# Optimization experiments

Measured on AMD Instinct MI355X. Metric: run time of the kernel, lower is better.

The kernel has to match this reference:

```python
import jax, jax.numpy as jnp
import numpy as np

ES = 256
NUM_SPECIES, NUM_ABILITIES, NUM_ITEMS, NUM_MOVES = 1026, 300, 500, 920
NUM_ITEM_EFFECTS, NUM_GENDERS, NUM_STATUS, NUM_VOLATILE_STATUS = 16, 3, 8, 105
B, N, F = 8192, 12, 42
# feature layout (flat int32 vector per entity)
(SPECIES, ABILITY, ITEM, ITEM_EFFECT, GENDER, STATUS, BEING_CALLED_BACK, TRAPPED,
 NEWLY_SWITCHED, TOXIC_TURNS, SLEEP_TURNS, FAINTED, ACTIVE, SIDE, LEVEL, HP, MAXHP) = range(17)
BOOST0, VOL0, MOVEID0, MOVEPP0 = 17, 24, 33, 37  # 7 boosts, 9 volatile words, 4 moves, 4 pp

DENSE_DIMS = [("hp", 10), ("level", 7), ("active", 2), ("onehot", 32), ("boosts", 7),
              ("volatiles", NUM_VOLATILE_STATUS), ("item", ES + NUM_ITEM_EFFECTS),
              ("side", 2), ("moves", ES + 6)]

def _bits(x, world_dim):
    # binary-scale embedding: bit decomposition of an int feature
    nb = (world_dim - 1).bit_length()
    mask = jnp.asarray(1 << np.arange(nb), dtype=jnp.int32)
    return ((x[..., None] & mask) != 0).astype(jnp.float32)

def setup_inputs() -> dict:
    key = jax.random.key(0)
    ks = jax.random.split(key, 32)
    s = 0.02
    inp = {"entities": jax.random.randint(ks[0], (B, N, F), 0, 2, dtype=jnp.int32)}
    inp["embed_species"] = jax.random.normal(ks[1], (NUM_SPECIES, ES), jnp.float32) * s
    inp["embed_ability"] = jax.random.normal(ks[2], (NUM_ABILITIES, ES), jnp.float32) * s
    inp["embed_item"] = jax.random.normal(ks[3], (NUM_ITEMS, ES), jnp.float32) * s
    inp["embed_moves"] = jax.random.normal(ks[4], (NUM_MOVES, ES), jnp.float32) * s
    for i, (name, din) in enumerate(DENSE_DIMS):
        inp[f"{name}_W"] = jax.random.normal(ks[5 + i], (din, ES), jnp.float32) * s
        inp[f"{name}_b"] = jnp.zeros((ES,), jnp.float32)
    return inp

def _forward(entities, embed_species, embed_ability, embed_item, embed_moves,
             hp_W, hp_b, level_W, level_b, active_W, active_b, onehot_W, onehot_b,
             boosts_W, boosts_b, volatiles_W, volatiles_b, item_W, item_b,
             side_W, side_b, moves_W, moves_b):
    e = entities
    oh = jax.nn.one_hot
    dense = lambda x, W, b: x @ W + b
    hp = e[..., HP].astype(jnp.float32)
    maxhp = jnp.clip(e[..., MAXHP], 1).astype(jnp.float32)
    hp_ratio = jnp.clip(hp / maxhp, 0.0, 1.0)                      # (B,N)
    hp_token = jnp.floor(1023.0 * hp_ratio).astype(jnp.int32)
    boolean_code = jnp.concatenate([
        hp_ratio[..., None], oh(e[..., GENDER], NUM_GENDERS), oh(e[..., STATUS], NUM_STATUS),
        oh(e[..., BEING_CALLED_BACK], 2), oh(e[..., TRAPPED], 2), oh(e[..., NEWLY_SWITCHED], 2),
        oh(e[..., TOXIC_TURNS], 8), oh(e[..., SLEEP_TURNS], 4), oh(e[..., FAINTED], 2)], axis=-1)  # (B,N,32)
    item_onehot = jnp.concatenate([embed_item[e[..., ITEM]], oh(e[..., ITEM_EFFECT], NUM_ITEM_EFFECTS)], axis=-1)
    boosts = e[..., BOOST0:VOL0].astype(jnp.float32) / 2.0          # (B,N,7)
    vol = e[..., VOL0:VOL0 + 9]
    vbits = (vol[..., None] & jnp.arange(16)) > 0                   # (B,N,9,16)
    vol_oh = vbits.reshape(*vol.shape[:-1], 144)[..., :NUM_VOLATILE_STATUS].astype(jnp.float32)
    moveset = jnp.concatenate([embed_moves[e[..., MOVEID0:MOVEPP0]],
                               _bits(e[..., MOVEPP0:MOVEPP0 + 4], 64)], axis=-1)  # (B,N,4,262)
    moves_out = jnp.einsum('bnmf,fd->bnd', moveset, moves_W) + 4.0 * moves_b      # sum of 4 Dense outputs
    emb = (dense(_bits(hp_token, 1024), hp_W, hp_b)
           + dense(_bits(e[..., LEVEL], 101), level_W, level_b)
           + dense(oh(e[..., ACTIVE], 2), active_W, active_b)
           + dense(boolean_code, onehot_W, onehot_b)
           + dense(boosts, boosts_W, boosts_b)
           + dense(vol_oh, volatiles_W, volatiles_b)
           + embed_species[e[..., SPECIES]]
           + embed_ability[e[..., ABILITY]]
           + dense(item_onehot, item_W, item_b)
           + dense(oh(e[..., SIDE], 2), side_W, side_b)
           + moves_out)
    return emb

def reference(entities, embed_species, embed_ability, embed_item, embed_moves,
              hp_W, hp_b, level_W, level_b, active_W, active_b, onehot_W, onehot_b,
              boosts_W, boosts_b, volatiles_W, volatiles_b, item_W, item_b,
              side_W, side_b, moves_W, moves_b):
    return _forward(entities, embed_species, embed_ability, embed_item, embed_moves,
                    hp_W, hp_b, level_W, level_b, active_W, active_b, onehot_W, onehot_b,
                    boosts_W, boosts_b, volatiles_W, volatiles_b, item_W, item_b,
                    side_W, side_b, moves_W, moves_b)
```

## Files before the change

kernel.cpp:

```cpp
#include <hip/hip_runtime.h>

#define ES 256
#define B_DIM 8192
#define N_DIM 12
#define NFEAT 42
#define NENT (B_DIM * N_DIM)

#define F_SPECIES 0
#define F_ABILITY 1
#define F_ITEM 2
#define F_ITEM_EFFECT 3
#define F_GENDER 4
#define F_STATUS 5
#define F_BCB 6
#define F_TRAPPED 7
#define F_NEWSW 8
#define F_TOXIC 9
#define F_SLEEP 10
#define F_FAINTED 11
#define F_ACTIVE 12
#define F_SIDE 13
#define F_LEVEL 14
#define F_HP 15
#define F_MAXHP 16
#define F_BOOST0 17
#define F_VOL0 24
#define F_MOVEID0 33
#define F_MOVEPP0 37

#define OFF_HP     0
#define OFF_LV     (OFF_HP + 1024*ES)
#define OFF_PP     (OFF_LV + 128*ES)
#define OFF_VP     (OFF_PP + 64*ES)
#define OFF_CA     (OFF_VP + 784*ES)
#define OFF_CB     (OFF_CA + 768*ES)
#define OFF_EITEM  (OFF_CB + 1024*ES)
#define OFF_EMOVES (OFF_EITEM + 500*ES)
#define WS_FLOATS  (OFF_EMOVES + 920*ES)

#define TB_HP0 0
#define TB_LV0 1024
#define TB_PP0 1152
#define TB_VP0 1216
#define TB_CA0 2000
#define TB_CB0 2768
#define TB_EI0 3792
#define TB_EM0 3917
#define TB_TOT 4147

__global__ __launch_bounds__(256) void k_tables(
    const float* __restrict__ item_e, const float* __restrict__ moves_e,
    const float* __restrict__ hp_W, const float* __restrict__ level_W,
    const float* __restrict__ moves_W, const float* __restrict__ vol_W,
    const float* __restrict__ item_W, const float* __restrict__ onehot_W,
    const float* __restrict__ active_W, const float* __restrict__ side_W,
    const float* __restrict__ hp_b, const float* __restrict__ level_b,
    const float* __restrict__ active_b, const float* __restrict__ onehot_b,
    const float* __restrict__ boosts_b, const float* __restrict__ vol_b,
    const float* __restrict__ item_b, const float* __restrict__ side_b,
    const float* __restrict__ moves_b,
    float* __restrict__ ws) {
    __shared__ float se[4][ES];
    int bid = blockIdx.x;
    int d = threadIdx.x;

    if (bid < TB_LV0) {
        int v = bid;
        float acc = 0.f;
        for (int b = 0; b < 10; ++b)
            if ((v >> b) & 1) acc += hp_W[b * ES + d];
        ws[OFF_HP + v * ES + d] = acc;
    } else if (bid < TB_PP0) {
        int v = bid - TB_LV0;
        float acc = 0.f;
        for (int b = 0; b < 7; ++b)
            if ((v >> b) & 1) acc += level_W[b * ES + d];
        ws[OFF_LV + v * ES + d] = acc;
    } else if (bid < TB_VP0) {
        int v = bid - TB_PP0;
        float acc = 0.f;
        for (int b = 0; b < 6; ++b)
            if ((v >> b) & 1) acc += moves_W[(256 + b) * ES + d];
        ws[OFF_PP + v * ES + d] = acc;
    } else if (bid < TB_CA0) {
        int v = bid - TB_VP0;
        float acc = 0.f;
        if (v < 768) {
            int t = v >> 8, pair = v & 255, a = pair >> 4, b = pair & 15;
            for (int j = 0; j < 16; ++j) {
                if (a & j) acc += vol_W[(32 * t + j) * ES + d];
                if (b & j) acc += vol_W[(32 * t + 16 + j) * ES + d];
            }
        } else {
            int a = v - 768;
            for (int j = 0; j < 9; ++j)
                if (a & j) acc += vol_W[(96 + j) * ES + d];
        }
        ws[OFF_VP + v * ES + d] = acc;
    } else if (bid < TB_CB0) {
        int idx = bid - TB_CA0;
        int fa = idx & 1, ns = (idx >> 1) & 1, tr = (idx >> 2) & 1, bcb = (idx >> 3) & 1;
        int rest = idx >> 4, g = rest % 3, e = rest / 3;
        ws[OFF_CA + idx * ES + d] =
            item_W[(256 + e) * ES + d] + onehot_W[(1 + g) * ES + d] +
            onehot_W[(12 + bcb) * ES + d] + onehot_W[(14 + tr) * ES + d] +
            onehot_W[(16 + ns) * ES + d] + onehot_W[(30 + fa) * ES + d];
    } else if (bid < TB_EI0) {
        int idx = bid - TB_CB0;
        int sd = idx & 1, act = (idx >> 1) & 1, sl = (idx >> 2) & 3,
            tox = (idx >> 4) & 7, st = idx >> 7;
        float bias = hp_b[d] + level_b[d] + active_b[d] + onehot_b[d] + boosts_b[d] +
                     vol_b[d] + item_b[d] + side_b[d] + 4.0f * moves_b[d];
        ws[OFF_CB + idx * ES + d] =
            bias + onehot_W[(4 + st) * ES + d] + onehot_W[(18 + tox) * ES + d] +
            onehot_W[(26 + sl) * ES + d] + active_W[act * ES + d] + side_W[sd * ES + d];
    } else {
        const float* E; const float* W; float* o; int r0;
        if (bid < TB_EM0) { E = item_e;  W = item_W;  o = ws + OFF_EITEM;  r0 = (bid - TB_EI0) * 4; }
        else              { E = moves_e; W = moves_W; o = ws + OFF_EMOVES; r0 = (bid - TB_EM0) * 4; }
        for (int i = d; i < 4 * ES; i += 256)
            se[i >> 8][i & 255] = E[(r0 + (i >> 8)) * ES + (i & 255)];
        __syncthreads();
        int rl = d >> 6, lane = d & 63, d0 = lane * 4;
        float4 acc = make_float4(0.f, 0.f, 0.f, 0.f);
#pragma unroll 4
        for (int k = 0; k < ES; ++k) {
            float e = se[rl][k];
            const float4 w = *reinterpret_cast<const float4*>(&W[k * ES + d0]);
            acc.x += e * w.x; acc.y += e * w.y; acc.z += e * w.z; acc.w += e * w.w;
        }
        *reinterpret_cast<float4*>(&o[(r0 + rl) * ES + d0]) = acc;
    }
}


__device__ __forceinline__ float4 ld4(const float* p) {
    return *reinterpret_cast<const float4*>(p);
}
__device__ __forceinline__ void add4(float4& a, const float4 b) {
    a.x += b.x; a.y += b.y; a.z += b.z; a.w += b.w;
}
__device__ __forceinline__ void fma4(float4& a, float s, const float4 b) {
    a.x += s * b.x; a.y += s * b.y; a.z += s * b.z; a.w += s * b.w;
}
__device__ __forceinline__ int sclamp(int x, int lo, int hi) {
    return x < lo ? lo : (x > hi ? hi : x);
}

__global__ __launch_bounds__(256) void k_main(
    const int* __restrict__ ent,
    const float* __restrict__ spW, const float* __restrict__ abW,
    const float* __restrict__ onehotW, const float* __restrict__ boostsW,
    const float* __restrict__ ws,
    float* __restrict__ out) {
    int lane = threadIdx.x & 63;
    int wid  = (blockIdx.x * 256 + threadIdx.x) >> 6;
    int went = __builtin_amdgcn_readfirstlane(wid);
    int d0 = lane * 4;

    int fv = ent[went * NFEAT + (lane < NFEAT ? lane : 0)];
#define RL(i) __builtin_amdgcn_readlane(fv, (i))

    const float* Hp     = ws + OFF_HP;
    const float* Lv     = ws + OFF_LV;
    const float* Pp     = ws + OFF_PP;
    const float* VP     = ws + OFF_VP;
    const float* CA     = ws + OFF_CA;
    const float* CB     = ws + OFF_CB;
    const float* Eitem  = ws + OFF_EITEM;
    const float* Emoves = ws + OFF_EMOVES;

    int idxB = ((((RL(F_STATUS) & 7) * 8 + (RL(F_TOXIC) & 7)) * 4 + (RL(F_SLEEP) & 3)) * 2 +
                (RL(F_ACTIVE) & 1)) * 2 + (RL(F_SIDE) & 1);
    float4 acc = ld4(CB + idxB * ES + d0);

    int g = sclamp(RL(F_GENDER), 0, 2);
    int idxA = (((((RL(F_ITEM_EFFECT) & 15) * 3 + g) * 2 + (RL(F_BCB) & 1)) * 2 +
                 (RL(F_TRAPPED) & 1)) * 2 + (RL(F_NEWSW) & 1)) * 2 + (RL(F_FAINTED) & 1);
    add4(acc, ld4(CA + idxA * ES + d0));

    add4(acc, ld4(spW    + sclamp(RL(F_SPECIES), 0, 1025) * ES + d0));
    add4(acc, ld4(abW    + sclamp(RL(F_ABILITY), 0, 299)  * ES + d0));
    add4(acc, ld4(Eitem  + sclamp(RL(F_ITEM),    0, 499)  * ES + d0));

    {
        float hp = (float)RL(F_HP);
        int mh = RL(F_MAXHP); if (mh < 1) mh = 1;
        float ratio = fminf(fmaxf(hp / (float)mh, 0.f), 1.f);
        int tok = __builtin_amdgcn_readfirstlane((int)floorf(1023.f * ratio));
        add4(acc, ld4(Hp + tok * ES + d0));
        fma4(acc, ratio, ld4(onehotW + d0));
    }

    add4(acc, ld4(Lv + (RL(F_LEVEL) & 127) * ES + d0));

#pragma unroll
    for (int k = 0; k < 7; ++k) {
        int bv = RL(F_BOOST0 + k);
        if (bv != 0) fma4(acc, 0.5f * (float)bv, ld4(boostsW + k * ES + d0));
    }

#pragma unroll
    for (int t = 0; t < 3; ++t) {
        int pair = ((RL(F_VOL0 + 2 * t) & 15) << 4) | (RL(F_VOL0 + 2 * t + 1) & 15);
        if (pair != 0) add4(acc, ld4(VP + (t * 256 + pair) * ES + d0));
    }
    {
        int nib = RL(F_VOL0 + 6) & 15;
        if (nib != 0) add4(acc, ld4(VP + (768 + nib) * ES + d0));
    }

#pragma unroll
    for (int m = 0; m < 4; ++m) {
        add4(acc, ld4(Emoves + sclamp(RL(F_MOVEID0 + m), 0, 919) * ES + d0));
        int pp = RL(F_MOVEPP0 + m) & 63;
        if (pp != 0) add4(acc, ld4(Pp + pp * ES + d0));
    }
#undef RL

    *reinterpret_cast<float4*>(&out[went * ES + d0]) = acc;
}


extern "C" void kernel_launch(void* const* d_in, const int* in_sizes, int n_in,
                              void* d_out, int out_size, void* d_ws, size_t ws_size,
                              hipStream_t stream) {
    const int*   entities = (const int*)  d_in[0];
    const float* sp       = (const float*)d_in[1];
    const float* ab       = (const float*)d_in[2];
    const float* item_e   = (const float*)d_in[3];
    const float* moves_e  = (const float*)d_in[4];
    const float* hp_W     = (const float*)d_in[5];
    const float* hp_b     = (const float*)d_in[6];
    const float* level_W  = (const float*)d_in[7];
    const float* level_b  = (const float*)d_in[8];
    const float* active_W = (const float*)d_in[9];
    const float* active_b = (const float*)d_in[10];
    const float* onehot_W = (const float*)d_in[11];
    const float* onehot_b = (const float*)d_in[12];
    const float* boosts_W = (const float*)d_in[13];
    const float* boosts_b = (const float*)d_in[14];
    const float* vol_W    = (const float*)d_in[15];
    const float* vol_b    = (const float*)d_in[16];
    const float* item_W   = (const float*)d_in[17];
    const float* item_b   = (const float*)d_in[18];
    const float* side_W   = (const float*)d_in[19];
    const float* side_b   = (const float*)d_in[20];
    const float* moves_W  = (const float*)d_in[21];
    const float* moves_b  = (const float*)d_in[22];

    float* ws  = (float*)d_ws;
    float* out = (float*)d_out;

    k_tables<<<TB_TOT, 256, 0, stream>>>(item_e, moves_e, hp_W, level_W, moves_W, vol_W,
                                         item_W, onehot_W, active_W, side_W,
                                         hp_b, level_b, active_b, onehot_b, boosts_b,
                                         vol_b, item_b, side_b, moves_b, ws);

    k_main<<<NENT / 4, 256, 0, stream>>>(entities, sp, ab, onehot_W, boosts_W, ws, out);
}
```

Measured before the change: 260.5 us.

## Issue all gather loads up front, vectorize table build, nontemporal output stores

The main kernel now computes every table index first, then issues all gather loads unconditionally before summing them in a tree. Previously the loads were interleaved with branches, so many more independent memory requests can be in flight per wave. Rows for zero volatile pairs, zero pp values and zero boosts are simply loaded and added, which relies on those table rows being zero or scaled by zero. The table-precompute kernel handles four rows per block with float4 loads and stores, cutting its block count. The output is written with nontemporal stores to avoid polluting the cache.

```diff
diff --git a/kernel.cpp b/kernel.cpp
--- a/kernel.cpp
+++ b/kernel.cpp
@@ -1,10 +1,8 @@
 #include <hip/hip_runtime.h>
 
 #define ES 256
-#define B_DIM 8192
-#define N_DIM 12
 #define NFEAT 42
-#define NENT (B_DIM * N_DIM)
+#define NENT (8192 * 12)
 
 #define F_SPECIES 0
 #define F_ABILITY 1
@@ -36,17 +34,41 @@
 #define OFF_CB     (OFF_CA + 768*ES)
 #define OFF_EITEM  (OFF_CB + 1024*ES)
 #define OFF_EMOVES (OFF_EITEM + 500*ES)
-#define WS_FLOATS  (OFF_EMOVES + 920*ES)
+
+typedef float vf4 __attribute__((ext_vector_type(4)));
+
+__device__ __forceinline__ float4 ld4(const float* p) {
+    return *reinterpret_cast<const float4*>(p);
+}
+__device__ __forceinline__ void st4(float* p, const float4 v) {
+    *reinterpret_cast<float4*>(p) = v;
+}
+__device__ __forceinline__ void st4_nt(float* p, const float4 v) {
+    vf4 t = {v.x, v.y, v.z, v.w};
+    __builtin_nontemporal_store(t, reinterpret_cast<vf4*>(p));
+}
+__device__ __forceinline__ void add4(float4& a, const float4 b) {
+    a.x += b.x; a.y += b.y; a.z += b.z; a.w += b.w;
+}
+__device__ __forceinline__ float4 sum4(const float4 a, const float4 b) {
+    return make_float4(a.x + b.x, a.y + b.y, a.z + b.z, a.w + b.w);
+}
+__device__ __forceinline__ void fma4(float4& a, float s, const float4 b) {
+    a.x += s * b.x; a.y += s * b.y; a.z += s * b.z; a.w += s * b.w;
+}
+__device__ __forceinline__ int sclamp(int x, int lo, int hi) {
+    return x < lo ? lo : (x > hi ? hi : x);
+}
 
 #define TB_HP0 0
-#define TB_LV0 1024
-#define TB_PP0 1152
-#define TB_VP0 1216
-#define TB_CA0 2000
-#define TB_CB0 2768
-#define TB_EI0 3792
-#define TB_EM0 3917
-#define TB_TOT 4147
+#define TB_LV0 256
+#define TB_PP0 288
+#define TB_VP0 304
+#define TB_CA0 500
+#define TB_CB0 692
+#define TB_EI0 948
+#define TB_EM0 1073
+#define TB_TOT 1303
 
 __global__ __launch_bounds__(256) void k_tables(
     const float* __restrict__ item_e, const float* __restrict__ moves_e,
@@ -60,92 +82,79 @@
     const float* __restrict__ item_b, const float* __restrict__ side_b,
     const float* __restrict__ moves_b,
     float* __restrict__ ws) {
-    __shared__ float se[4][ES];
-    int bid = blockIdx.x;
-    int d = threadIdx.x;
+    __shared__ float4 se4[4][64];
+    const int bid = blockIdx.x, tid = threadIdx.x;
+    const int rl = tid >> 6, lane = tid & 63, d0 = lane * 4;
+    float4 acc = make_float4(0.f, 0.f, 0.f, 0.f);
 
     if (bid < TB_LV0) {
-        int v = bid;
-        float acc = 0.f;
+        int v = (bid - TB_HP0) * 4 + rl;
         for (int b = 0; b < 10; ++b)
-            if ((v >> b) & 1) acc += hp_W[b * ES + d];
-        ws[OFF_HP + v * ES + d] = acc;
+            if ((v >> b) & 1) add4(acc, ld4(hp_W + b * ES + d0));
+        st4(ws + OFF_HP + v * ES + d0, acc);
     } else if (bid < TB_PP0) {
-        int v = bid - TB_LV0;
-        float acc = 0.f;
+        int v = (bid - TB_LV0) * 4 + rl;
         for (int b = 0; b < 7; ++b)
-            if ((v >> b) & 1) acc += level_W[b * ES + d];
-        ws[OFF_LV + v * ES + d] = acc;
+            if ((v >> b) & 1) add4(acc, ld4(level_W + b * ES + d0));
+        st4(ws + OFF_LV + v * ES + d0, acc);
     } else if (bid < TB_VP0) {
-        int v = bid - TB_PP0;
-        float acc = 0.f;
+        int v = (bid - TB_PP0) * 4 + rl;
         for (int b = 0; b < 6; ++b)
-            if ((v >> b) & 1) acc += moves_W[(256 + b) * ES + d];
-        ws[OFF_PP + v * ES + d] = acc;
+            if ((v >> b) & 1) add4(acc, ld4(moves_W + (256 + b) * ES + d0));
+        st4(ws + OFF_PP + v * ES + d0, acc);
     } else if (bid < TB_CA0) {
-        int v = bid - TB_VP0;
-        float acc = 0.f;
+        int v = (bid - TB_VP0) * 4 + rl;
         if (v < 768) {
             int t = v >> 8, pair = v & 255, a = pair >> 4, b = pair & 15;
             for (int j = 0; j < 16; ++j) {
-                if (a & j) acc += vol_W[(32 * t + j) * ES + d];
-                if (b & j) acc += vol_W[(32 * t + 16 + j) * ES + d];
+                if (a & j) add4(acc, ld4(vol_W + (32 * t + j) * ES + d0));
+                if (b & j) add4(acc, ld4(vol_W + (32 * t + 16 + j) * ES + d0));
             }
         } else {
             int a = v - 768;
             for (int j = 0; j < 9; ++j)
-                if (a & j) acc += vol_W[(96 + j) * ES + d];
+                if (a & j) add4(acc, ld4(vol_W + (96 + j) * ES + d0));
         }
-        ws[OFF_VP + v * ES + d] = acc;
+        st4(ws + OFF_VP + v * ES + d0, acc);
     } else if (bid < TB_CB0) {
-        int idx = bid - TB_CA0;
+        int idx = (bid - TB_CA0) * 4 + rl;
         int fa = idx & 1, ns = (idx >> 1) & 1, tr = (idx >> 2) & 1, bcb = (idx >> 3) & 1;
         int rest = idx >> 4, g = rest % 3, e = rest / 3;
-        ws[OFF_CA + idx * ES + d] =
-            item_W[(256 + e) * ES + d] + onehot_W[(1 + g) * ES + d] +
-            onehot_W[(12 + bcb) * ES + d] + onehot_W[(14 + tr) * ES + d] +
-            onehot_W[(16 + ns) * ES + d] + onehot_W[(30 + fa) * ES + d];
+        acc = sum4(sum4(ld4(item_W + (256 + e) * ES + d0), ld4(onehot_W + (1 + g) * ES + d0)),
+                   sum4(ld4(onehot_W + (12 + bcb) * ES + d0), ld4(onehot_W + (14 + tr) * ES + d0)));
+        add4(acc, sum4(ld4(onehot_W + (16 + ns) * ES + d0), ld4(onehot_W + (30 + fa) * ES + d0)));
+        st4(ws + OFF_CA + idx * ES + d0, acc);
     } else if (bid < TB_EI0) {
-        int idx = bid - TB_CB0;
+        int idx = (bid - TB_CB0) * 4 + rl;
         int sd = idx & 1, act = (idx >> 1) & 1, sl = (idx >> 2) & 3,
             tox = (idx >> 4) & 7, st = idx >> 7;
-        float bias = hp_b[d] + level_b[d] + active_b[d] + onehot_b[d] + boosts_b[d] +
-                     vol_b[d] + item_b[d] + side_b[d] + 4.0f * moves_b[d];
-        ws[OFF_CB + idx * ES + d] =
-            bias + onehot_W[(4 + st) * ES + d] + onehot_W[(18 + tox) * ES + d] +
-            onehot_W[(26 + sl) * ES + d] + active_W[act * ES + d] + side_W[sd * ES + d];
+        acc = sum4(sum4(ld4(hp_b + d0), ld4(level_b + d0)),
+                   sum4(ld4(active_b + d0), ld4(onehot_b + d0)));
+        add4(acc, sum4(ld4(boosts_b + d0), ld4(vol_b + d0)));
+        add4(acc, sum4(ld4(item_b + d0), ld4(side_b + d0)));
+        fma4(acc, 4.0f, ld4(moves_b + d0));
+        add4(acc, sum4(ld4(onehot_W + (4 + st) * ES + d0), ld4(onehot_W + (18 + tox) * ES + d0)));
+        add4(acc, sum4(ld4(onehot_W + (26 + sl) * ES + d0),
+                       sum4(ld4(active_W + act * ES + d0), ld4(side_W + sd * ES + d0))));
+        st4(ws + OFF_CB + idx * ES + d0, acc);
     } else {
         const float* E; const float* W; float* o; int r0;
         if (bid < TB_EM0) { E = item_e;  W = item_W;  o = ws + OFF_EITEM;  r0 = (bid - TB_EI0) * 4; }
         else              { E = moves_e; W = moves_W; o = ws + OFF_EMOVES; r0 = (bid - TB_EM0) * 4; }
-        for (int i = d; i < 4 * ES; i += 256)
-            se[i >> 8][i & 255] = E[(r0 + (i >> 8)) * ES + (i & 255)];
+        se4[tid >> 6][tid & 63] = ld4(E + r0 * ES + tid * 4);
         __syncthreads();
-        int rl = d >> 6, lane = d & 63, d0 = lane * 4;
-        float4 acc = make_float4(0.f, 0.f, 0.f, 0.f);
 #pragma unroll 4
-        for (int k = 0; k < ES; ++k) {
-            float e = se[rl][k];
-            const float4 w = *reinterpret_cast<const float4*>(&W[k * ES + d0]);
-            acc.x += e * w.x; acc.y += e * w.y; acc.z += e * w.z; acc.w += e * w.w;
+        for (int k0 = 0; k0 < 64; ++k0) {
+            float4 e4 = se4[rl][k0];
+            fma4(acc, e4.x, ld4(W + (4 * k0 + 0) * ES + d0));
+            fma4(acc, e4.y, ld4(W + (4 * k0 + 1) * ES + d0));
+            fma4(acc, e4.z, ld4(W + (4 * k0 + 2) * ES + d0));
+            fma4(acc, e4.w, ld4(W + (4 * k0 + 3) * ES + d0));
         }
-        *reinterpret_cast<float4*>(&o[(r0 + rl) * ES + d0]) = acc;
+        st4(o + (r0 + rl) * ES + d0, acc);
     }
 }
 
-
-__device__ __forceinline__ float4 ld4(const float* p) {
-    return *reinterpret_cast<const float4*>(p);
-}
-__device__ __forceinline__ void add4(float4& a, const float4 b) {
-    a.x += b.x; a.y += b.y; a.z += b.z; a.w += b.w;
-}
-__device__ __forceinline__ void fma4(float4& a, float s, const float4 b) {
-    a.x += s * b.x; a.y += s * b.y; a.z += s * b.z; a.w += s * b.w;
-}
-__device__ __forceinline__ int sclamp(int x, int lo, int hi) {
-    return x < lo ? lo : (x > hi ? hi : x);
-}
 
 __global__ __launch_bounds__(256) void k_main(
     const int* __restrict__ ent,
@@ -153,10 +162,9 @@
     const float* __restrict__ onehotW, const float* __restrict__ boostsW,
     const float* __restrict__ ws,
     float* __restrict__ out) {
-    int lane = threadIdx.x & 63;
-    int wid  = (blockIdx.x * 256 + threadIdx.x) >> 6;
-    int went = __builtin_amdgcn_readfirstlane(wid);
-    int d0 = lane * 4;
+    const int lane = threadIdx.x & 63;
+    const int went = __builtin_amdgcn_readfirstlane((blockIdx.x * 256 + threadIdx.x) >> 6);
+    const int d0 = lane * 4;
 
     int fv = ent[went * NFEAT + (lane < NFEAT ? lane : 0)];
 #define RL(i) __builtin_amdgcn_readlane(fv, (i))
@@ -170,55 +178,77 @@
     const float* Eitem  = ws + OFF_EITEM;
     const float* Emoves = ws + OFF_EMOVES;
 
-    int idxB = ((((RL(F_STATUS) & 7) * 8 + (RL(F_TOXIC) & 7)) * 4 + (RL(F_SLEEP) & 3)) * 2 +
-                (RL(F_ACTIVE) & 1)) * 2 + (RL(F_SIDE) & 1);
-    float4 acc = ld4(CB + idxB * ES + d0);
-
-    int g = sclamp(RL(F_GENDER), 0, 2);
-    int idxA = (((((RL(F_ITEM_EFFECT) & 15) * 3 + g) * 2 + (RL(F_BCB) & 1)) * 2 +
-                 (RL(F_TRAPPED) & 1)) * 2 + (RL(F_NEWSW) & 1)) * 2 + (RL(F_FAINTED) & 1);
-    add4(acc, ld4(CA + idxA * ES + d0));
-
-    add4(acc, ld4(spW    + sclamp(RL(F_SPECIES), 0, 1025) * ES + d0));
-    add4(acc, ld4(abW    + sclamp(RL(F_ABILITY), 0, 299)  * ES + d0));
-    add4(acc, ld4(Eitem  + sclamp(RL(F_ITEM),    0, 499)  * ES + d0));
-
-    {
-        float hp = (float)RL(F_HP);
-        int mh = RL(F_MAXHP); if (mh < 1) mh = 1;
-        float ratio = fminf(fmaxf(hp / (float)mh, 0.f), 1.f);
-        int tok = __builtin_amdgcn_readfirstlane((int)floorf(1023.f * ratio));
-        add4(acc, ld4(Hp + tok * ES + d0));
-        fma4(acc, ratio, ld4(onehotW + d0));
-    }
-
-    add4(acc, ld4(Lv + (RL(F_LEVEL) & 127) * ES + d0));
-
-#pragma unroll
-    for (int k = 0; k < 7; ++k) {
-        int bv = RL(F_BOOST0 + k);
-        if (bv != 0) fma4(acc, 0.5f * (float)bv, ld4(boostsW + k * ES + d0));
-    }
-
-#pragma unroll
-    for (int t = 0; t < 3; ++t) {
-        int pair = ((RL(F_VOL0 + 2 * t) & 15) << 4) | (RL(F_VOL0 + 2 * t + 1) & 15);
-        if (pair != 0) add4(acc, ld4(VP + (t * 256 + pair) * ES + d0));
-    }
-    {
-        int nib = RL(F_VOL0 + 6) & 15;
-        if (nib != 0) add4(acc, ld4(VP + (768 + nib) * ES + d0));
-    }
-
-#pragma unroll
-    for (int m = 0; m < 4; ++m) {
-        add4(acc, ld4(Emoves + sclamp(RL(F_MOVEID0 + m), 0, 919) * ES + d0));
-        int pp = RL(F_MOVEPP0 + m) & 63;
-        if (pp != 0) add4(acc, ld4(Pp + pp * ES + d0));
-    }
+    const int iB = ((((RL(F_STATUS) & 7) * 8 + (RL(F_TOXIC) & 7)) * 4 + (RL(F_SLEEP) & 3)) * 2 +
+                    (RL(F_ACTIVE) & 1)) * 2 + (RL(F_SIDE) & 1);
+    const int iA = (((((RL(F_ITEM_EFFECT) & 15) * 3 + sclamp(RL(F_GENDER), 0, 2)) * 2 +
+                      (RL(F_BCB) & 1)) * 2 + (RL(F_TRAPPED) & 1)) * 2 +
+                    (RL(F_NEWSW) & 1)) * 2 + (RL(F_FAINTED) & 1);
+    const int iSP = sclamp(RL(F_SPECIES), 0, 1025);
+    const int iAB = sclamp(RL(F_ABILITY), 0, 299);
+    const int iIT = sclamp(RL(F_ITEM), 0, 499);
+    const float hp = (float)RL(F_HP);
+    int mh = RL(F_MAXHP); if (mh < 1) mh = 1;
+    const float ratio = fminf(fmaxf(hp / (float)mh, 0.f), 1.f);
+    const int tok = __builtin_amdgcn_readfirstlane((int)floorf(1023.f * ratio));
+    const int iLV = RL(F_LEVEL) & 127;
+    const int b0 = RL(F_BOOST0 + 0), b1 = RL(F_BOOST0 + 1), b2 = RL(F_BOOST0 + 2),
+              b3 = RL(F_BOOST0 + 3), b4 = RL(F_BOOST0 + 4), b5 = RL(F_BOOST0 + 5),
+              b6 = RL(F_BOOST0 + 6);
+    const int vp0 = ((RL(F_VOL0 + 0) & 15) << 4) | (RL(F_VOL0 + 1) & 15);
+    const int vp1 = ((RL(F_VOL0 + 2) & 15) << 4) | (RL(F_VOL0 + 3) & 15);
+    const int vp2 = ((RL(F_VOL0 + 4) & 15) << 4) | (RL(F_VOL0 + 5) & 15);
+    const int v6  = RL(F_VOL0 + 6) & 15;
+    const int m0 = sclamp(RL(F_MOVEID0 + 0), 0, 919), m1 = sclamp(RL(F_MOVEID0 + 1), 0, 919),
+              m2 = sclamp(RL(F_MOVEID0 + 2), 0, 919), m3 = sclamp(RL(F_MOVEID0 + 3), 0, 919);
+    const int p0 = RL(F_MOVEPP0 + 0) & 63, p1 = RL(F_MOVEPP0 + 1) & 63,
+              p2 = RL(F_MOVEPP0 + 2) & 63, p3 = RL(F_MOVEPP0 + 3) & 63;
 #undef RL
 
-    *reinterpret_cast<float4*>(&out[went * ES + d0]) = acc;
+    const float4 xCB  = ld4(CB + iB * ES + d0);
+    const float4 xCA  = ld4(CA + iA * ES + d0);
+    const float4 xSP  = ld4(spW + iSP * ES + d0);
+    const float4 xAB  = ld4(abW + iAB * ES + d0);
+    const float4 xIT  = ld4(Eitem + iIT * ES + d0);
+    const float4 xHP  = ld4(Hp + tok * ES + d0);
+    const float4 xOH  = ld4(onehotW + d0);
+    const float4 xLV  = ld4(Lv + iLV * ES + d0);
+    const float4 xV0  = ld4(VP + (0 * 256 + vp0) * ES + d0);
+    const float4 xV1  = ld4(VP + (1 * 256 + vp1) * ES + d0);
+    const float4 xV2  = ld4(VP + (2 * 256 + vp2) * ES + d0);
+    const float4 xV6  = ld4(VP + (768 + v6) * ES + d0);
+    const float4 xE0  = ld4(Emoves + m0 * ES + d0);
+    const float4 xE1  = ld4(Emoves + m1 * ES + d0);
+    const float4 xE2  = ld4(Emoves + m2 * ES + d0);
+    const float4 xE3  = ld4(Emoves + m3 * ES + d0);
+    const float4 xP0  = ld4(Pp + p0 * ES + d0);
+    const float4 xP1  = ld4(Pp + p1 * ES + d0);
+    const float4 xP2  = ld4(Pp + p2 * ES + d0);
+    const float4 xP3  = ld4(Pp + p3 * ES + d0);
+    const float4 xB0  = ld4(boostsW + 0 * ES + d0);
+    const float4 xB1  = ld4(boostsW + 1 * ES + d0);
+    const float4 xB2  = ld4(boostsW + 2 * ES + d0);
+    const float4 xB3  = ld4(boostsW + 3 * ES + d0);
+    const float4 xB4  = ld4(boostsW + 4 * ES + d0);
+    const float4 xB5  = ld4(boostsW + 5 * ES + d0);
+    const float4 xB6  = ld4(boostsW + 6 * ES + d0);
+
+    float4 s0 = sum4(sum4(xCB, xCA), sum4(xSP, xAB));
+    float4 s1 = sum4(sum4(xIT, xHP), sum4(xLV, xV6));
+    float4 s2 = sum4(sum4(xV0, xV1), sum4(xV2, xE0));
+    float4 s3 = sum4(sum4(xE1, xE2), sum4(xE3, xP0));
+    float4 s4 = sum4(sum4(xP1, xP2), xP3);
+    float4 acc = sum4(sum4(s0, s1), sum4(s2, s3));
+    add4(acc, s4);
+    fma4(acc, ratio, xOH);
+    fma4(acc, 0.5f * (float)b0, xB0);
+    fma4(acc, 0.5f * (float)b1, xB1);
+    fma4(acc, 0.5f * (float)b2, xB2);
+    fma4(acc, 0.5f * (float)b3, xB3);
+    fma4(acc, 0.5f * (float)b4, xB4);
+    fma4(acc, 0.5f * (float)b5, xB5);
+    fma4(acc, 0.5f * (float)b6, xB6);
+
+    st4_nt(out + went * ES + d0, acc);
 }
 
 
```

After: 251.3 us. 3.5% less time.
